# Kernel optimization log

Hardware: AMD Instinct MI355X
Metric: run time of the kernel (lower is better)

## Reference

```python
import jax, jax.numpy as jnp
import numpy as np
import math

D_MODEL, N_HEADS, N_LEVELS, N_POINTS = 256, 8, 4, 4
SPATIAL = [(80, 80), (40, 40), (20, 20), (10, 10)]


def setup_inputs() -> dict:
    key = jax.random.key(0)
    ks = jax.random.split(key, 8)
    N = 1
    C, H, L, P = D_MODEL, N_HEADS, N_LEVELS, N_POINTS
    shapes = np.array(SPATIAL, np.int32)
    len_in = int((shapes[:, 0] * shapes[:, 1]).sum())  # 8500
    Lq = len_in  # encoder self-attention: queries == flattened pixels
    start = np.concatenate([[0], np.cumsum(shapes[:, 0] * shapes[:, 1])[:-1]]).astype(np.int32)

    query = jax.random.normal(ks[0], (N, Lq, C), jnp.float32)
    reference_points = jax.random.uniform(ks[1], (N, Lq, L, 2), dtype=jnp.float32)
    input_flatten = jax.random.normal(ks[2], (N, len_in, C), jnp.float32)

    # sampling_offsets bias: grid init as in _reset_parameters
    thetas = jnp.arange(H, dtype=jnp.float32) * (2.0 * math.pi / H)
    grid = jnp.stack([jnp.cos(thetas), jnp.sin(thetas)], -1)
    grid = grid / jnp.max(jnp.abs(grid), axis=-1, keepdims=True)
    grid = jnp.tile(grid[:, None, None, :], (1, L, P, 1)) * jnp.arange(1, P + 1, dtype=jnp.float32)[None, None, :, None]
    b_off = grid.reshape(-1)
    W_off = jax.random.normal(ks[3], (C, H * L * P * 2), jnp.float32) * 0.01
    W_attn = jax.random.normal(ks[4], (C, H * L * P), jnp.float32) * 0.01
    b_attn = jnp.zeros((H * L * P,), jnp.float32)
    s = 1.0 / np.sqrt(C)
    W_v = jax.random.normal(ks[5], (C, C), jnp.float32) * s
    b_v = jnp.zeros((C,), jnp.float32)
    W_out = jax.random.normal(ks[6], (C, C), jnp.float32) * s
    b_out = jnp.zeros((C,), jnp.float32)
    return {
        "query": query, "reference_points": reference_points, "input_flatten": input_flatten,
        "input_spatial_shapes": jnp.asarray(shapes), "input_level_start_index": jnp.asarray(start),
        "W_off": W_off, "b_off": b_off, "W_attn": W_attn, "b_attn": b_attn,
        "W_v": W_v, "b_v": b_v, "W_out": W_out, "b_out": b_out,
    }


def _ms_deform_core(value, spatial_shapes, level_start_index, loc, attn):
    # value: (N, Len_in, H, d); loc: (N, Lq, H, L, P, 2) normalized [0,1]; attn: (N, Lq, H, L, P)
    N, Len_in, H, d = value.shape
    _, Lq, _, L, P, _ = loc.shape
    Hi = spatial_shapes[:, 0][None, None, None, :, None]  # (1,1,1,L,1)
    Wi = spatial_shapes[:, 1][None, None, None, :, None]
    # grid_sample(align_corners=False) semantics used by the CUDA ms_deform_attn kernel
    x = loc[..., 0] * Wi.astype(loc.dtype) - 0.5  # (N,Lq,H,L,P)
    y = loc[..., 1] * Hi.astype(loc.dtype) - 0.5
    x0 = jnp.floor(x); y0 = jnp.floor(y)
    lw = x - x0; lh = y - y0
    x0i = x0.astype(jnp.int32); y0i = y0.astype(jnp.int32)
    v = value.transpose(0, 2, 1, 3)  # (N,H,Len_in,d)
    start = level_start_index[None, None, None, :, None]
    out = jnp.zeros((N, Lq, H, d), value.dtype)
    corners = [(0, 0, (1 - lh) * (1 - lw)), (0, 1, (1 - lh) * lw),
               (1, 0, lh * (1 - lw)), (1, 1, lh * lw)]
    for dy, dx, wgt in corners:
        hc = y0i + dy; wc = x0i + dx
        valid = (hc >= 0) & (hc < Hi) & (wc >= 0) & (wc < Wi)
        idx = start + jnp.clip(hc, 0, Hi - 1) * Wi + jnp.clip(wc, 0, Wi - 1)  # (N,Lq,H,L,P)
        w = jnp.where(valid, wgt, 0.0) * attn  # (N,Lq,H,L,P)
        idx_g = idx.transpose(0, 2, 1, 3, 4).reshape(N, H, Lq * L * P)
        sampled = jnp.take_along_axis(v, idx_g[..., None], axis=2)  # (N,H,Lq*L*P,d)
        sampled = sampled.reshape(N, H, Lq, L, P, d)
        out = out + jnp.einsum('nhqlpd,nqhlp->nqhd', sampled, w)
    return out.reshape(N, Lq, H * d)


def reference(query, reference_points, input_flatten, input_spatial_shapes, input_level_start_index,
              W_off, b_off, W_attn, b_attn, W_v, b_v, W_out, b_out):
    N, Lq, C = query.shape
    H, L, P = N_HEADS, N_LEVELS, N_POINTS
    d = C // H
    value = (input_flatten @ W_v + b_v).reshape(N, -1, H, d)
    off = (query @ W_off + b_off).reshape(N, Lq, H, L, P, 2)
    attn = jax.nn.softmax((query @ W_attn + b_attn).reshape(N, Lq, H, L * P), axis=-1)
    attn = attn.reshape(N, Lq, H, L, P)
    # reference_points last dim == 2 branch
    norm = jnp.stack([input_spatial_shapes[:, 1], input_spatial_shapes[:, 0]], -1).astype(query.dtype)  # (L,2) = (W,H)
    loc = reference_points[:, :, None, :, None, :] + off / norm[None, None, None, :, None, :]
    out = _ms_deform_core(value, input_spatial_shapes, input_level_start_index, loc, attn)
    return out @ W_out + b_out
```

## Files before the change

### kernel.cpp

```cpp
#include <hip/hip_runtime.h>

#define LQ    8500
#define C_DIM 256

typedef __attribute__((ext_vector_type(8))) short bf16x8;
typedef __attribute__((ext_vector_type(4))) float f32x4;

__device__ __forceinline__ unsigned short f2bf(float x) {
    union { float f; unsigned u; } c; c.f = x;
    unsigned r = c.u + 0x7FFFu + ((c.u >> 16) & 1u);
    return (unsigned short)(r >> 16);
}
__device__ __forceinline__ float bf2f(unsigned us) {
    union { unsigned u; float f; } c; c.u = us << 16;
    return c.f;
}

__device__ __forceinline__ void gload_lds16(const void* g, void* l) {
    __builtin_amdgcn_global_load_lds(
        (const __attribute__((address_space(1))) unsigned int*)g,
        (__attribute__((address_space(3))) unsigned int*)l, 16, 0, 0);
}

__global__ __launch_bounds__(256)
void prep_all(const float* __restrict__ query, const float* __restrict__ inflat,
              const float* __restrict__ Wv,   const float* __restrict__ Wout,
              const float* __restrict__ Woff, const float* __restrict__ Wattn,
              const float* __restrict__ boff, const float* __restrict__ battn,
              unsigned short* __restrict__ qbf,  unsigned short* __restrict__ ibf,
              unsigned short* __restrict__ Wv_t, unsigned short* __restrict__ Wout_t,
              unsigned short* __restrict__ Wcat_t, float* __restrict__ bcat)
{
    const int NV = LQ * 256 / 8;
    const int tid    = blockIdx.x * 256 + threadIdx.x;
    const int stride = gridDim.x * 256;

    for (int v = tid; v < 2 * NV; v += stride) {
        const float*    src = (v < NV) ? query + (size_t)v * 8 : inflat + (size_t)(v - NV) * 8;
        unsigned short* dst = (v < NV) ? qbf   + (size_t)v * 8 : ibf    + (size_t)(v - NV) * 8;
        const float4 f0 = ((const float4*)src)[0];
        const float4 f1 = ((const float4*)src)[1];
        bf16x8 o;
        o[0] = (short)f2bf(f0.x); o[1] = (short)f2bf(f0.y);
        o[2] = (short)f2bf(f0.z); o[3] = (short)f2bf(f0.w);
        o[4] = (short)f2bf(f1.x); o[5] = (short)f2bf(f1.y);
        o[6] = (short)f2bf(f1.z); o[7] = (short)f2bf(f1.w);
        *(bf16x8*)dst = o;
    }

    const int total = 65536 * 3 + 32768 + 384;
    for (int i = tid; i < total; i += stride) {
        if (i < 65536) {
            int k = i >> 8, n = i & 255;
            Wv_t[n * 256 + k] = f2bf(Wv[i]);
        } else if (i < 131072) {
            int j = i - 65536; int k = j >> 8, n = j & 255;
            Wout_t[n * 256 + k] = f2bf(Wout[j]);
        } else if (i < 196608) {
            int j = i - 131072; int k = j >> 8, n = j & 255;
            Wcat_t[n * 256 + k] = f2bf(Woff[j]);
        } else if (i < 229376) {
            int j = i - 196608; int k = j >> 7, n = j & 127;
            Wcat_t[(256 + n) * 256 + k] = f2bf(Wattn[j]);
        } else {
            int j = i - 229376;
            bcat[j] = (j < 256) ? boff[j] : battn[j - 256];
        }
    }
}

template<int OUTMODE>
__device__ __forceinline__ void gemm_body(
    const unsigned short* __restrict__ A, const unsigned short* __restrict__ Bt,
    const float* __restrict__ bias, void* __restrict__ Out,
    int M, int N, int r0, int c0,
    char* As, char* Bs)
{
    const int t    = threadIdx.x;
    const int lane = t & 63, wave = t >> 6;
    const int wr   = wave >> 1, wc = wave & 1;
    const int lrow = lane & 15, lgrp = lane >> 4;

    f32x4 acc[2][2] = {{{}, {}}, {{}, {}}};

    auto stage = [&](int buf, int k0) {
#pragma unroll
        for (int r = 0; r < 2; ++r) {
            const int row   = r * 32 + (t >> 3);
            const int chunk = (t & 7) ^ (row & 7);
            const unsigned short* g =
                A + (size_t)min(r0 + row, M - 1) * 256 + k0 + chunk * 8;
            gload_lds16(g, As + buf * 8192 + r * 4096 + wave * 1024);
        }
#pragma unroll
        for (int r = 0; r < 2; ++r) {
            const int row   = r * 32 + (t >> 3);
            const int chunk = (t & 7) ^ (row & 7);
            const unsigned short* g = Bt + (size_t)(c0 + row) * 256 + k0 + chunk * 8;
            gload_lds16(g, Bs + buf * 8192 + r * 4096 + wave * 1024);
        }
    };

    auto compute = [&](int buf) {
#pragma unroll
        for (int kk = 0; kk < 2; ++kk) {
            const int g = kk * 4 + lgrp;
            bf16x8 a[2], b[2];
#pragma unroll
            for (int mi = 0; mi < 2; ++mi) {
                const int row = wr * 32 + mi * 16 + lrow;
                a[mi] = *(const bf16x8*)(As + buf * 8192 + row * 128 +
                                         ((g ^ (row & 7)) * 16));
            }
#pragma unroll
            for (int nj = 0; nj < 2; ++nj) {
                const int row = wc * 32 + nj * 16 + lrow;
                b[nj] = *(const bf16x8*)(Bs + buf * 8192 + row * 128 +
                                         ((g ^ (row & 7)) * 16));
            }
#pragma unroll
            for (int mi = 0; mi < 2; ++mi)
#pragma unroll
                for (int nj = 0; nj < 2; ++nj)
                    acc[mi][nj] = __builtin_amdgcn_mfma_f32_16x16x32_bf16(
                        a[mi], b[nj], acc[mi][nj], 0, 0, 0);
        }
    };

    stage(0, 0);
    __syncthreads();
    int cur = 0;
#pragma unroll
    for (int it = 0; it < 3; ++it) {
        stage(cur ^ 1, (it + 1) * 64);
        compute(cur);
        __syncthreads();
        cur ^= 1;
    }
    compute(cur);

#pragma unroll
    for (int mi = 0; mi < 2; ++mi)
#pragma unroll
        for (int nj = 0; nj < 2; ++nj) {
            const int col = c0 + wc * 32 + nj * 16 + lrow;
            const float bb = bias[col];
#pragma unroll
            for (int j = 0; j < 4; ++j) {
                const int row = r0 + wr * 32 + mi * 16 + lgrp * 4 + j;
                if (row < M) {
                    const float v = acc[mi][nj][j] + bb;
                    if constexpr (OUTMODE == 0)
                        ((float*)Out)[(size_t)row * N + col] = v;
                    else if constexpr (OUTMODE == 1)
                        ((unsigned short*)Out)[(size_t)row * N + col] = f2bf(v);
                    else
                        ((unsigned short*)Out)[(size_t)(col >> 5) * (LQ * 32) +
                                               (size_t)row * 32 + (col & 31)] = f2bf(v);
                }
            }
        }
}

__global__ __launch_bounds__(256)
void gemm_dual(const unsigned short* __restrict__ A0, const unsigned short* __restrict__ B0,
               const float* __restrict__ bias0, unsigned short* __restrict__ out0,
               const unsigned short* __restrict__ A1, const unsigned short* __restrict__ B1,
               const float* __restrict__ bias1, unsigned short* __restrict__ out1)
{
    __shared__ __align__(16) char As[2 * 64 * 64 * 2];
    __shared__ __align__(16) char Bs[2 * 64 * 64 * 2];
    const int y  = blockIdx.y;
    const int r0 = blockIdx.x * 64;
    if (y < 4)
        gemm_body<2>(A0, B0, bias0, out0, LQ, 256, r0, y * 64, As, Bs);
    else
        gemm_body<1>(A1, B1, bias1, out1, LQ, 384, r0, (y - 4) * 64, As, Bs);
}

__global__ __launch_bounds__(256)
void gemm_f32out(const unsigned short* __restrict__ A, const unsigned short* __restrict__ Bt,
                 const float* __restrict__ bias, float* __restrict__ out)
{
    __shared__ __align__(16) char As[2 * 64 * 64 * 2];
    __shared__ __align__(16) char Bs[2 * 64 * 64 * 2];
    gemm_body<0>(A, Bt, bias, out, LQ, 256, blockIdx.x * 64, blockIdx.y * 64,
                 As, Bs);
}

__global__ __launch_bounds__(256)
void msda_sample(const unsigned short* __restrict__ value,
                 const unsigned short* __restrict__ offattn,
                 const float* __restrict__ refp,
                 const int*   __restrict__ shapes,
                 const int*   __restrict__ lstart,
                 unsigned short* __restrict__ msda)
{
    __shared__ int   s_off[2][128][5];
    __shared__ float s_w[2][128][5];

    const int t   = threadIdx.x;
    const int sub = t >> 7, tl = t & 127;
    const int q   = blockIdx.x * 2 + sub;

    {
        const int lp = tl & 15, l = lp >> 2;
        const int Hs = shapes[2 * l + 0];
        const int Ws = shapes[2 * l + 1];
        const int st = lstart[l];

        const unsigned oxy = *(const unsigned*)(offattn + (size_t)q * 384 + 2 * tl);
        const float ox = bf2f(oxy & 0xffffu);
        const float oy = bf2f(oxy >> 16);
        const float rx = refp[q * 8 + l * 2 + 0];
        const float ry = refp[q * 8 + l * 2 + 1];

        const float x = (rx + ox / (float)Ws) * (float)Ws - 0.5f;
        const float y = (ry + oy / (float)Hs) * (float)Hs - 0.5f;
        const float x0f = floorf(x), y0f = floorf(y);
        const float lw = x - x0f, lh = y - y0f;
        const int   x0 = (int)x0f, y0 = (int)y0f;

        const float logit = bf2f(offattn[(size_t)q * 384 + 256 + tl]);
        float m = logit;
        for (int s = 8; s >= 1; s >>= 1) m = fmaxf(m, __shfl_xor(m, s, 16));
        const float e = __expf(logit - m);
        float ssum = e;
        for (int s = 8; s >= 1; s >>= 1) ssum += __shfl_xor(ssum, s, 16);
        const float a = e / ssum;

#pragma unroll
        for (int corner = 0; corner < 4; ++corner) {
            const int dy = corner >> 1, dx = corner & 1;
            const int hc = y0 + dy, wc = x0 + dx;
            const bool valid = (hc >= 0) && (hc < Hs) && (wc >= 0) && (wc < Ws);
            const float wy = dy ? lh : (1.f - lh);
            const float wx = dx ? lw : (1.f - lw);
            const int hcc = min(max(hc, 0), Hs - 1);
            const int wcc = min(max(wc, 0), Ws - 1);
            s_off[sub][tl][corner] = (st + hcc * Ws + wcc) * 64;
            s_w[sub][tl][corner]   = valid ? (wy * wx * a) : 0.f;
        }
    }
    __syncthreads();

    const int chunk = tl & 3, quarter = (tl >> 2) & 3, h = tl >> 4;
    const char* vb = (const char*)value + (size_t)h * (LQ * 64) + chunk * 16;
    float a0 = 0.f, a1 = 0.f, a2 = 0.f, a3 = 0.f;
    float a4 = 0.f, a5 = 0.f, a6 = 0.f, a7 = 0.f;
#pragma unroll
    for (int j = 0; j < 4; ++j) {
        const int c = h * 16 + quarter * 4 + j;
#pragma unroll
        for (int corner = 0; corner < 4; ++corner) {
            const float w  = s_w[sub][c][corner];
            const int   bo = s_off[sub][c][corner];
            const uint4 v = *(const uint4*)(vb + (size_t)(unsigned)bo);
            a0 = fmaf(w, bf2f(v.x & 0xffffu), a0);
            a1 = fmaf(w, bf2f(v.x >> 16), a1);
            a2 = fmaf(w, bf2f(v.y & 0xffffu), a2);
            a3 = fmaf(w, bf2f(v.y >> 16), a3);
            a4 = fmaf(w, bf2f(v.z & 0xffffu), a4);
            a5 = fmaf(w, bf2f(v.z >> 16), a5);
            a6 = fmaf(w, bf2f(v.w & 0xffffu), a6);
            a7 = fmaf(w, bf2f(v.w >> 16), a7);
        }
    }
    a0 += __shfl_xor(a0, 4); a0 += __shfl_xor(a0, 8);
    a1 += __shfl_xor(a1, 4); a1 += __shfl_xor(a1, 8);
    a2 += __shfl_xor(a2, 4); a2 += __shfl_xor(a2, 8);
    a3 += __shfl_xor(a3, 4); a3 += __shfl_xor(a3, 8);
    a4 += __shfl_xor(a4, 4); a4 += __shfl_xor(a4, 8);
    a5 += __shfl_xor(a5, 4); a5 += __shfl_xor(a5, 8);
    a6 += __shfl_xor(a6, 4); a6 += __shfl_xor(a6, 8);
    a7 += __shfl_xor(a7, 4); a7 += __shfl_xor(a7, 8);
    if (quarter == 0) {
        uint4 o;
        o.x = (unsigned)f2bf(a0) | ((unsigned)f2bf(a1) << 16);
        o.y = (unsigned)f2bf(a2) | ((unsigned)f2bf(a3) << 16);
        o.z = (unsigned)f2bf(a4) | ((unsigned)f2bf(a5) << 16);
        o.w = (unsigned)f2bf(a6) | ((unsigned)f2bf(a7) << 16);
        *(uint4*)(msda + (size_t)q * 256 + h * 32 + chunk * 8) = o;
    }
}

extern "C" void kernel_launch(void* const* d_in, const int* in_sizes, int n_in,
                              void* d_out, int out_size, void* d_ws, size_t ws_size,
                              hipStream_t stream)
{
    const float* query  = (const float*)d_in[0];
    const float* refp   = (const float*)d_in[1];
    const float* inflat = (const float*)d_in[2];
    const int*   shapes = (const int*)  d_in[3];
    const int*   lstart = (const int*)  d_in[4];
    const float* W_off  = (const float*)d_in[5];
    const float* b_off  = (const float*)d_in[6];
    const float* W_attn = (const float*)d_in[7];
    const float* b_attn = (const float*)d_in[8];
    const float* W_v    = (const float*)d_in[9];
    const float* b_v    = (const float*)d_in[10];
    const float* W_out  = (const float*)d_in[11];
    const float* b_out  = (const float*)d_in[12];

    float* out = (float*)d_out;
    char*  ws  = (char*)d_ws;

    size_t o = 0;
    unsigned short* qbf    = (unsigned short*)(ws + o); o += (size_t)LQ * 256 * 2;
    unsigned short* ibf    = (unsigned short*)(ws + o); o += (size_t)LQ * 256 * 2;
    unsigned short* Wv_t   = (unsigned short*)(ws + o); o += 131072;
    unsigned short* Wout_t = (unsigned short*)(ws + o); o += 131072;
    unsigned short* Wcat_t = (unsigned short*)(ws + o); o += 196608;
    float*          bcat   = (float*)         (ws + o); o += 1536;
    unsigned short* value  = (unsigned short*)(ws + o); o += (size_t)LQ * 256 * 2;
    unsigned short* offattn= (unsigned short*)(ws + o); o += (size_t)LQ * 384 * 2;
    unsigned short* msda   = (unsigned short*)(ws + o);

    prep_all<<<1024, 256, 0, stream>>>(query, inflat, W_v, W_out, W_off, W_attn,
                                       b_off, b_attn, qbf, ibf,
                                       Wv_t, Wout_t, Wcat_t, bcat);

    gemm_dual<<<dim3(133, 10), 256, 0, stream>>>(ibf, Wv_t, b_v, value,
                                                 qbf, Wcat_t, bcat, offattn);

    msda_sample<<<4250, 256, 0, stream>>>(value, offattn, refp, shapes, lstart, msda);

    gemm_f32out<<<dim3(133, 4), 256, 0, stream>>>(msda, Wout_t, b_out, out);
}
```

Measured before the change: 54.42 us.

## Fuse fp32-to-bf16 activation conversion into the first GEMM's A-tile load

Measured after the change: 58.28 us. 1.07x slower.

```diff
diff --git a/kernel.cpp b/kernel.cpp
--- a/kernel.cpp
+++ b/kernel.cpp
@@ -23,33 +23,14 @@
 }
 
 __global__ __launch_bounds__(256)
-void prep_all(const float* __restrict__ query, const float* __restrict__ inflat,
-              const float* __restrict__ Wv,   const float* __restrict__ Wout,
-              const float* __restrict__ Woff, const float* __restrict__ Wattn,
-              const float* __restrict__ boff, const float* __restrict__ battn,
-              unsigned short* __restrict__ qbf,  unsigned short* __restrict__ ibf,
-              unsigned short* __restrict__ Wv_t, unsigned short* __restrict__ Wout_t,
-              unsigned short* __restrict__ Wcat_t, float* __restrict__ bcat)
-{
-    const int NV = LQ * 256 / 8;
-    const int tid    = blockIdx.x * 256 + threadIdx.x;
-    const int stride = gridDim.x * 256;
-
-    for (int v = tid; v < 2 * NV; v += stride) {
-        const float*    src = (v < NV) ? query + (size_t)v * 8 : inflat + (size_t)(v - NV) * 8;
-        unsigned short* dst = (v < NV) ? qbf   + (size_t)v * 8 : ibf    + (size_t)(v - NV) * 8;
-        const float4 f0 = ((const float4*)src)[0];
-        const float4 f1 = ((const float4*)src)[1];
-        bf16x8 o;
-        o[0] = (short)f2bf(f0.x); o[1] = (short)f2bf(f0.y);
-        o[2] = (short)f2bf(f0.z); o[3] = (short)f2bf(f0.w);
-        o[4] = (short)f2bf(f1.x); o[5] = (short)f2bf(f1.y);
-        o[6] = (short)f2bf(f1.z); o[7] = (short)f2bf(f1.w);
-        *(bf16x8*)dst = o;
-    }
-
+void prep_w(const float* __restrict__ Wv,   const float* __restrict__ Wout,
+            const float* __restrict__ Woff, const float* __restrict__ Wattn,
+            const float* __restrict__ boff, const float* __restrict__ battn,
+            unsigned short* __restrict__ Wv_t, unsigned short* __restrict__ Wout_t,
+            unsigned short* __restrict__ Wcat_t, float* __restrict__ bcat)
+{
     const int total = 65536 * 3 + 32768 + 384;
-    for (int i = tid; i < total; i += stride) {
+    for (int i = blockIdx.x * 256 + threadIdx.x; i < total; i += gridDim.x * 256) {
         if (i < 65536) {
             int k = i >> 8, n = i & 255;
             Wv_t[n * 256 + k] = f2bf(Wv[i]);
@@ -69,9 +50,9 @@
     }
 }
 
-template<int OUTMODE>
+template<int OUTMODE, bool A_F32>
 __device__ __forceinline__ void gemm_body(
-    const unsigned short* __restrict__ A, const unsigned short* __restrict__ Bt,
+    const void* __restrict__ Av, const unsigned short* __restrict__ Bt,
     const float* __restrict__ bias, void* __restrict__ Out,
     int M, int N, int r0, int c0,
     char* As, char* Bs)
@@ -82,21 +63,46 @@
     const int lrow = lane & 15, lgrp = lane >> 4;
 
     f32x4 acc[2][2] = {{{}, {}}, {{}, {}}};
-
-    auto stage = [&](int buf, int k0) {
+    float4 fa[2][2];
+
+    auto loadA = [&](int buf, int k0) {
 #pragma unroll
         for (int r = 0; r < 2; ++r) {
-            const int row   = r * 32 + (t >> 3);
-            const int chunk = (t & 7) ^ (row & 7);
-            const unsigned short* g =
-                A + (size_t)min(r0 + row, M - 1) * 256 + k0 + chunk * 8;
-            gload_lds16(g, As + buf * 8192 + r * 4096 + wave * 1024);
-        }
+            const int rr = r * 32 + (t >> 3);
+            if constexpr (A_F32) {
+                const float* g = (const float*)Av +
+                                 (size_t)min(r0 + rr, M - 1) * 256 + k0 + (t & 7) * 8;
+                fa[r][0] = ((const float4*)g)[0];
+                fa[r][1] = ((const float4*)g)[1];
+            } else {
+                const int chunk = (t & 7) ^ (rr & 7);
+                const unsigned short* g = (const unsigned short*)Av +
+                                          (size_t)min(r0 + rr, M - 1) * 256 + k0 + chunk * 8;
+                gload_lds16(g, As + buf * 8192 + r * 4096 + wave * 1024);
+            }
+        }
+    };
+    auto writeA = [&](int buf) {
+        if constexpr (A_F32) {
+#pragma unroll
+            for (int r = 0; r < 2; ++r) {
+                const int rr = r * 32 + (t >> 3);
+                bf16x8 o;
+                o[0] = (short)f2bf(fa[r][0].x); o[1] = (short)f2bf(fa[r][0].y);
+                o[2] = (short)f2bf(fa[r][0].z); o[3] = (short)f2bf(fa[r][0].w);
+                o[4] = (short)f2bf(fa[r][1].x); o[5] = (short)f2bf(fa[r][1].y);
+                o[6] = (short)f2bf(fa[r][1].z); o[7] = (short)f2bf(fa[r][1].w);
+                *(bf16x8*)(As + buf * 8192 + rr * 128 +
+                           (((t & 7) ^ (rr & 7)) * 16)) = o;
+            }
+        }
+    };
+    auto loadB = [&](int buf, int k0) {
 #pragma unroll
         for (int r = 0; r < 2; ++r) {
-            const int row   = r * 32 + (t >> 3);
-            const int chunk = (t & 7) ^ (row & 7);
-            const unsigned short* g = Bt + (size_t)(c0 + row) * 256 + k0 + chunk * 8;
+            const int rr = r * 32 + (t >> 3);
+            const int chunk = (t & 7) ^ (rr & 7);
+            const unsigned short* g = Bt + (size_t)(c0 + rr) * 256 + k0 + chunk * 8;
             gload_lds16(g, Bs + buf * 8192 + r * 4096 + wave * 1024);
         }
     };
@@ -127,13 +133,15 @@
         }
     };
 
-    stage(0, 0);
+    loadA(0, 0); loadB(0, 0); writeA(0);
     __syncthreads();
     int cur = 0;
 #pragma unroll
     for (int it = 0; it < 3; ++it) {
-        stage(cur ^ 1, (it + 1) * 64);
+        loadA(cur ^ 1, (it + 1) * 64);
+        loadB(cur ^ 1, (it + 1) * 64);
         compute(cur);
+        writeA(cur ^ 1);
         __syncthreads();
         cur ^= 1;
     }
@@ -163,9 +171,9 @@
 }
 
 __global__ __launch_bounds__(256)
-void gemm_dual(const unsigned short* __restrict__ A0, const unsigned short* __restrict__ B0,
+void gemm_dual(const float* __restrict__ A0, const unsigned short* __restrict__ B0,
                const float* __restrict__ bias0, unsigned short* __restrict__ out0,
-               const unsigned short* __restrict__ A1, const unsigned short* __restrict__ B1,
+               const float* __restrict__ A1, const unsigned short* __restrict__ B1,
                const float* __restrict__ bias1, unsigned short* __restrict__ out1)
 {
     __shared__ __align__(16) char As[2 * 64 * 64 * 2];
@@ -173,9 +181,9 @@
     const int y  = blockIdx.y;
     const int r0 = blockIdx.x * 64;
     if (y < 4)
-        gemm_body<2>(A0, B0, bias0, out0, LQ, 256, r0, y * 64, As, Bs);
+        gemm_body<2, true>(A0, B0, bias0, out0, LQ, 256, r0, y * 64, As, Bs);
     else
-        gemm_body<1>(A1, B1, bias1, out1, LQ, 384, r0, (y - 4) * 64, As, Bs);
+        gemm_body<1, true>(A1, B1, bias1, out1, LQ, 384, r0, (y - 4) * 64, As, Bs);
 }
 
 __global__ __launch_bounds__(256)
@@ -184,8 +192,8 @@
 {
     __shared__ __align__(16) char As[2 * 64 * 64 * 2];
     __shared__ __align__(16) char Bs[2 * 64 * 64 * 2];
-    gemm_body<0>(A, Bt, bias, out, LQ, 256, blockIdx.x * 64, blockIdx.y * 64,
-                 As, Bs);
+    gemm_body<0, false>(A, Bt, bias, out, LQ, 256, blockIdx.x * 64, blockIdx.y * 64,
+                        As, Bs);
 }
 
 __global__ __launch_bounds__(256)
@@ -306,8 +314,6 @@
     char*  ws  = (char*)d_ws;
 
     size_t o = 0;
-    unsigned short* qbf    = (unsigned short*)(ws + o); o += (size_t)LQ * 256 * 2;
-    unsigned short* ibf    = (unsigned short*)(ws + o); o += (size_t)LQ * 256 * 2;
     unsigned short* Wv_t   = (unsigned short*)(ws + o); o += 131072;
     unsigned short* Wout_t = (unsigned short*)(ws + o); o += 131072;
     unsigned short* Wcat_t = (unsigned short*)(ws + o); o += 196608;
@@ -316,12 +322,11 @@
     unsigned short* offattn= (unsigned short*)(ws + o); o += (size_t)LQ * 384 * 2;
     unsigned short* msda   = (unsigned short*)(ws + o);
 
-    prep_all<<<1024, 256, 0, stream>>>(query, inflat, W_v, W_out, W_off, W_attn,
-                                       b_off, b_attn, qbf, ibf,
-                                       Wv_t, Wout_t, Wcat_t, bcat);
-
-    gemm_dual<<<dim3(133, 10), 256, 0, stream>>>(ibf, Wv_t, b_v, value,
-                                                 qbf, Wcat_t, bcat, offattn);
+    prep_w<<<128, 256, 0, stream>>>(W_v, W_out, W_off, W_attn, b_off, b_attn,
+                                    Wv_t, Wout_t, Wcat_t, bcat);
+
+    gemm_dual<<<dim3(133, 10), 256, 0, stream>>>(inflat, Wv_t, b_v, value,
+                                                 query, Wcat_t, bcat, offattn);
 
     msda_sample<<<4250, 256, 0, stream>>>(value, offattn, refp, shapes, lstart, msda);
 
```
